# Performance work log

Measured on AMD Instinct MI355X. Metric: run time of the kernel, lower is better.

## Reference

```python
import jax, jax.numpy as jnp
import numpy as np

EPS = 2e-5
NCG = 51  # int(64 / 1.25)

def _conv1d(x, w, d):
    # x: [B,C,L], w: [Co,Ci,K]; dilated 1D conv, SAME padding
    return jax.lax.conv_general_dilated(x, w, window_strides=(1,), padding='SAME',
                                        rhs_dilation=(d,), dimension_numbers=('NCH', 'OIH', 'NCH'))

def _lift(x, w, n_h=9):
    # GConvRdG: lift R1 -> R1xR+; scale h=2^s realized as kernel dilation, 1/h normalization
    return jnp.stack([_conv1d(x, w, 2 ** s) / (2.0 ** s) for s in range(n_h)], axis=2)

def _gg(x, w):
    # GConvGG on [B,C,H,L]; w: [Co,Ci,Nk,K]; h_crop: H_out = H - Nk + 1.
    # Output scale s mixes input scales s..s+Nk-1, each with spatial dilation 2^(s+i).
    Nk, H = w.shape[2], x.shape[2]
    outs = []
    for s in range(H - Nk + 1):
        acc = None
        for i in range(Nk):
            d = 2 ** (s + i)
            t = _conv1d(x[:, :, s + i, :], w[:, :, i, :], d) / float(d)
            acc = t if acc is None else acc + t
        outs.append(acc)
    return jnp.stack(outs, axis=2)

def _bn(x, g, b):
    # training-mode BatchNorm2d over [B,C,H,L], per-channel stats
    m = jnp.mean(x, axis=(0, 2, 3), keepdims=True)
    v = jnp.var(x, axis=(0, 2, 3), keepdims=True)
    return (x - m) * jax.lax.rsqrt(v + EPS) * g[None, :, None, None] + b[None, :, None, None]

def _pool4(x):
    # max_pooling_R1: kernel 4 stride 4 over spatial axis
    B, C, H, L = x.shape
    return jnp.max(x.reshape(B, C, H, L // 4, 4), axis=-1)

def _forward(x, w1, w2, w3, w4, w5, w6, w7, w8, w9, w10, w11,
             g1, b1, g2, b2, g3, b3, g4, b4, g5, b5, g6, b6, g7, b7, g8, b8, g9, b9, g10, b10):
    r = jax.nn.relu
    out = _lift(x, w1)                      # [B,51,9,L]
    out = _pool4(out)
    out = r(_bn(out, g1, b1))
    out = _pool4(out)
    out = r(_bn(_gg(out, w2), g2, b2))      # H 9->7
    out = r(_bn(_gg(out, w3), g3, b3))
    out = _pool4(out)
    out = r(_bn(_gg(out, w4), g4, b4))      # 7->5
    out = r(_bn(_gg(out, w5), g5, b5))
    out = _pool4(out)
    out = r(_bn(_gg(out, w6), g6, b6))      # 5->3
    out = r(_bn(_gg(out, w7), g7, b7))
    out = r(_bn(_gg(out, w8), g8, b8))
    out = _pool4(out)
    out = r(_bn(_gg(out, w9), g9, b9))      # 3->1
    out = r(_bn(_gg(out, w10), g10, b10))
    out = jnp.mean(out, axis=-1, keepdims=True)   # global mean over space -> [B,408,1,1]
    out = _gg(out, w11)                     # 1x1 classifier -> [B,10,1,1]
    out = jnp.max(out, axis=-2)             # max over h axis -> [B,10,1]
    return out.reshape(out.shape[0], 10)

def setup_inputs():
    key = jax.random.key(0)
    ks = jax.random.split(key, 16)
    c = NCG
    def w(k, shape):
        fan_in = float(np.prod(shape[1:]))
        return jax.random.normal(k, shape, jnp.float32) * fan_in ** -0.5
    inp = {
        'x': jax.random.normal(ks[0], (8, 1, 32768), jnp.float32),
        'w1': w(ks[1], (c, 1, 79)),
        'w2': w(ks[2], (c, c, 3, 3)),
        'w3': w(ks[3], (c, c, 1, 3)),
        'w4': w(ks[4], (2 * c, c, 3, 3)),
        'w5': w(ks[5], (2 * c, 2 * c, 1, 3)),
        'w6': w(ks[6], (4 * c, 2 * c, 3, 3)),
        'w7': w(ks[7], (4 * c, 4 * c, 1, 3)),
        'w8': w(ks[8], (4 * c, 4 * c, 1, 3)),
        'w9': w(ks[9], (8 * c, 4 * c, 3, 3)),
        'w10': w(ks[10], (8 * c, 8 * c, 1, 3)),
        'w11': w(ks[11], (10, 8 * c, 1, 1)),
    }
    widths = [c, c, c, 2 * c, 2 * c, 4 * c, 4 * c, 4 * c, 8 * c, 8 * c]
    for i, cw in enumerate(widths, 1):
        inp['g%d' % i] = jnp.ones((cw,), jnp.float32)
        inp['b%d' % i] = jnp.zeros((cw,), jnp.float32)
    return inp

def reference(x, w1, w2, w3, w4, w5, w6, w7, w8, w9, w10, w11,
              g1, b1, g2, b2, g3, b3, g4, b4, g5, b5, g6, b6, g7, b7, g8, b8, g9, b9, g10, b10):
    return _forward(x, w1, w2, w3, w4, w5, w6, w7, w8, w9, w10, w11,
                    g1, b1, g2, b2, g3, b3, g4, b4, g5, b5, g6, b6, g7, b7, g8, b8, g9, b9, g10, b10)
```

## Files before the change

### kernel.cpp

```cpp
#include <hip/hip_runtime.h>
#include <hip/hip_bf16.h>

#define EPSBN 2e-5f

typedef __attribute__((ext_vector_type(8))) short short8v;
typedef __attribute__((ext_vector_type(4))) float f32x4;

__device__ inline unsigned short f2bf(float f) {
  unsigned u = __float_as_uint(f);
  unsigned r = (u + 0x7FFFu + ((u >> 16) & 1u)) >> 16;
  return (unsigned short)r;
}
__device__ inline float bf2f(unsigned short h) {
  return __uint_as_float(((unsigned)h) << 16);
}

template <int CTRL>
__device__ inline float dpp_radd(float v) {
  int r = __builtin_amdgcn_update_dpp(0, __float_as_int(v), CTRL, 0xf, 0xf,
                                      true);
  return v + __int_as_float(r);
}

constexpr int XPADL = 9984;
constexpr int XPADR = 14336;
constexpr int PROW = XPADL + 32768 + XPADR;

__global__ __launch_bounds__(256) void pad_x_kernel(const float* __restrict__ x,
                                                    unsigned* __restrict__ xp) {
  int i = blockIdx.x * 256 + threadIdx.x;
  if (i >= 8 * PROW) return;
  int b = i / PROW;
  int pos = i - b * PROW - XPADL;
  float v = (pos >= 0 && pos < 32768) ? x[b * 32768 + pos] : 0.f;
  unsigned u = __float_as_uint(v);
  unsigned h = u >> 16;
  float lof = v - __uint_as_float(u & 0xffff0000u);
  unsigned lo = __float_as_uint(lof) >> 16;
  xp[i] = (h << 16) | lo;
}

__global__ __launch_bounds__(256) void pad_pair_kernel(
    const unsigned* __restrict__ xp, unsigned* __restrict__ xpH,
    unsigned* __restrict__ xpL) {
  const int i = blockIdx.x * 256 + threadIdx.x;
  if (i >= PROW) return;
  const int sb = blockIdx.y;
  const int s = sb >> 3;
  const int b = sb & 7;
  const int d = 1 << s;
  const unsigned* row = xp + b * PROW;
  unsigned u0 = row[i];
  unsigned u1 = (i + d < PROW) ? row[i + d] : 0u;
  size_t o = (size_t)sb * PROW + i;
  xpH[o] = (u0 >> 16) | (u1 & 0xffff0000u);
  xpL[o] = (u0 & 0xffffu) | (u1 << 16);
}

__global__ __launch_bounds__(256) void pack_w1_kernel(
    const float* __restrict__ W, short* __restrict__ A) {
  int idx = blockIdx.x * 256 + threadIdx.x;
  if (idx >= 9 * 64 * 96) return;
  int s = idx / (64 * 96);
  int rem = idx - s * 64 * 96;
  int co = rem / 96;
  int k = rem - co * 96;
  float v = 0.f;
  if (co < 51 && k < 79)
    v = W[co * 79 + k] * __uint_as_float((unsigned)(127 - s) << 23);
  unsigned short hi = f2bf(v);
  unsigned short lo = f2bf(v - bf2f(hi));
  A[(size_t)s * 2 * 64 * 96 + co * 96 + k] = (short)hi;
  A[(size_t)s * 2 * 64 * 96 + 64 * 96 + co * 96 + k] = (short)lo;
}

__global__ __launch_bounds__(256) void lift_mfma_kernel(
    const unsigned* __restrict__ xpH, const unsigned* __restrict__ xpL,
    const short* __restrict__ Apk1, float* __restrict__ y1,
    float* __restrict__ part1) {
  constexpr int P = 104;
  const int bid = blockIdx.x;
  const int lc = (bid & 7) * 64 + (bid >> 3);
  const int s = blockIdx.y;
  const int b = blockIdx.z;
  const int d = 1 << s;
  const int l0 = lc * 64;
  const int tid = threadIdx.x;
  const int lane = tid & 63;
  const int quad = lane >> 4;
  const int n0 = lane & 15;
  const int wv = tid >> 6;
  const int coBase = wv * 16;

  __shared__ __align__(16) short Bh[64 * P];
  __shared__ __align__(16) short Bl[64 * P];
  __shared__ float sCh[2][64];

  const int nB = tid & 63;
  const int rowW = ((nB & 3) << 4) | (nB >> 2);
  const int swzW = (nB & 3) << 3;
  const int ogu = __builtin_amdgcn_readfirstlane(tid >> 6);
  const unsigned* xqH = xpH + (size_t)(s * 8 + b) * PROW + XPADL + l0;
  const unsigned* xqL = xpL + (size_t)(s * 8 + b) * PROW + XPADL + l0;

#pragma unroll
  for (int r = 0; r < 3; ++r) {
    const int kb = (ogu + 4 * r) * 8;
    const int base = (kb - 39) * d;
    uint4 ph, pl;
    ph.x = xqH[base + nB];
    ph.y = xqH[base + 2 * d + nB];
    ph.z = xqH[base + 4 * d + nB];
    ph.w = xqH[base + 6 * d + nB];
    pl.x = xqL[base + nB];
    pl.y = xqL[base + 2 * d + nB];
    pl.z = xqL[base + 4 * d + nB];
    pl.w = xqL[base + 6 * d + nB];
    *(uint4*)(Bh + rowW * P + (kb ^ swzW)) = ph;
    *(uint4*)(Bl + rowW * P + (kb ^ swzW)) = pl;
  }

  const short* ApkS = Apk1 + (size_t)s * 2 * 64 * 96;
  const short* arowH = ApkS + (coBase + n0) * 96;
  const short* arowL = arowH + 64 * 96;

  __syncthreads();

  f32x4 acc[4];
#pragma unroll
  for (int t = 0; t < 4; ++t) acc[t] = (f32x4){0.f, 0.f, 0.f, 0.f};

#pragma unroll
  for (int ks = 0; ks < 3; ++ks) {
    short8v ah = *(const short8v*)(arowH + ks * 32 + quad * 8);
    short8v al = *(const short8v*)(arowL + ks * 32 + quad * 8);
#pragma unroll
    for (int t = 0; t < 4; ++t) {
      const int n = n0 + 16 * t;
      const int off = (ks * 32 + quad * 8) ^ (t << 3);
      short8v bh = *(const short8v*)(Bh + n * P + off);
      short8v bl = *(const short8v*)(Bl + n * P + off);
      acc[t] = __builtin_amdgcn_mfma_f32_16x16x32_bf16(ah, bh, acc[t], 0, 0, 0);
      acc[t] = __builtin_amdgcn_mfma_f32_16x16x32_bf16(ah, bl, acc[t], 0, 0, 0);
      acc[t] = __builtin_amdgcn_mfma_f32_16x16x32_bf16(al, bh, acc[t], 0, 0, 0);
    }
  }

#pragma unroll
  for (int reg = 0; reg < 4; ++reg) {
    const int co = coBase + quad * 4 + reg;
    float po = fmaxf(fmaxf(acc[0][reg], acc[1][reg]),
                     fmaxf(acc[2][reg], acc[3][reg]));
    const bool valid = (co < 51);
    if (valid) {
      y1[(((size_t)b * 51 + co) * 9 + s) * 8192 + (l0 >> 2) + n0] = po;
    }
    float us = valid ? po : 0.f;
    float sq = us * us;
    us = dpp_radd<0x128>(us);
    sq = dpp_radd<0x128>(sq);
    us = dpp_radd<0x124>(us);
    sq = dpp_radd<0x124>(sq);
    us = dpp_radd<0x122>(us);
    sq = dpp_radd<0x122>(sq);
    us = dpp_radd<0x121>(us);
    sq = dpp_radd<0x121>(sq);
    if (n0 == 0) {
      sCh[0][co] = us;
      sCh[1][co] = sq;
    }
  }
  __syncthreads();
  if (tid < 51) {
    float* pp = part1 + (size_t)lc * 128;
    atomicAdd(&pp[tid], sCh[0][tid]);
    atomicAdd(&pp[64 + tid], sCh[1][tid]);
  }
}

__global__ __launch_bounds__(128) void reduce_stats1_kernel(
    const float* __restrict__ p, float* __restrict__ st) {
  const int t = threadIdx.x;
  if (t >= 102) return;
  const int k0 = blockIdx.x * 64;
  const int off = (t < 51) ? t : (64 + t - 51);
  float s = 0.f;
  for (int k = k0; k < k0 + 64; ++k) s += p[k * 128 + off];
  atomicAdd(&st[(t < 51) ? t : (512 + t - 51)], s);
}

__global__ __launch_bounds__(256) void stats_kernel(
    const float* __restrict__ Y, float* __restrict__ st, int C, int HL,
    int NS) {
  const int c = blockIdx.x, b = blockIdx.y, z = blockIdx.z;
  const int slice = HL / NS;
  const float* p = Y + ((size_t)b * C + c) * HL + (size_t)z * slice;
  float s = 0.f, q = 0.f;
  for (int i = threadIdx.x; i < slice; i += 256) {
    float v = p[i];
    s += v;
    q += v * v;
  }
#pragma unroll
  for (int off = 32; off > 0; off >>= 1) {
    s += __shfl_down(s, off, 64);
    q += __shfl_down(q, off, 64);
  }
  __shared__ float ls[4], lq[4];
  const int wid = threadIdx.x >> 6, lane = threadIdx.x & 63;
  if (lane == 0) { ls[wid] = s; lq[wid] = q; }
  __syncthreads();
  if (threadIdx.x == 0) {
    atomicAdd(&st[c], ls[0] + ls[1] + ls[2] + ls[3]);
    atomicAdd(&st[512 + c], lq[0] + lq[1] + lq[2] + lq[3]);
  }
}

__global__ __launch_bounds__(256) void reduce_parts_kernel(
    const float* __restrict__ p, float* __restrict__ y, int n, int stride,
    int ns) {
  int i = blockIdx.x * 256 + threadIdx.x;
  if (i >= n) return;
  float s = 0.f;
  for (int k = 0; k < ns; ++k) s += p[(size_t)k * stride + i];
  y[i] = s;
}

__global__ __launch_bounds__(256) void bnrelu_pool_kernel(
    const float* __restrict__ Y, const float* __restrict__ st,
    const float* __restrict__ g, const float* __restrict__ bb,
    float* __restrict__ Z, int C, int H, int Lin, float invN,
    unsigned int total) {
  unsigned int idx = blockIdx.x * 256u + threadIdx.x;
  if (idx >= total) return;
  const unsigned int Lo = (unsigned int)(Lin >> 2);
  unsigned int lo = idx % Lo;
  unsigned int r1 = idx / Lo;
  unsigned int h = r1 % (unsigned int)H;
  unsigned int r2 = r1 / (unsigned int)H;
  unsigned int c = r2 % (unsigned int)C;
  unsigned int b = r2 / (unsigned int)C;
  float m = st[c] * invN;
  float v = st[512 + c] * invN - m * m;
  float sc = g[c] * rsqrtf(v + EPSBN);
  float bi = bb[c] - m * sc;
  const float* p = Y + (((size_t)b * C + c) * H + h) * Lin + 4u * lo;
  float a0 = p[0] * sc + bi, a1 = p[1] * sc + bi;
  float a2 = p[2] * sc + bi, a3 = p[3] * sc + bi;
  float r = fmaxf(fmaxf(a0, a1), fmaxf(a2, a3));
  Z[idx] = fmaxf(r, 0.f);
}

__global__ __launch_bounds__(256) void bnrelu_pool_bf16_kernel(
    const float* __restrict__ Y, const float* __restrict__ st,
    const float* __restrict__ g, const float* __restrict__ bb,
    unsigned short* __restrict__ Z, int C, int H, int Lin, float invN,
    unsigned int total) {
  unsigned int idx = blockIdx.x * 256u + threadIdx.x;
  if (idx >= total) return;
  const unsigned int Lo = (unsigned int)(Lin >> 2);
  unsigned int lo = idx % Lo;
  unsigned int r1 = idx / Lo;
  unsigned int h = r1 % (unsigned int)H;
  unsigned int r2 = r1 / (unsigned int)H;
  unsigned int c = r2 % (unsigned int)C;
  unsigned int b = r2 / (unsigned int)C;
  float m = st[c] * invN;
  float v = st[512 + c] * invN - m * m;
  float sc = g[c] * rsqrtf(v + EPSBN);
  float bi = bb[c] - m * sc;
  const float* p = Y + (((size_t)b * C + c) * H + h) * Lin + 4u * lo;
  float a0 = p[0] * sc + bi, a1 = p[1] * sc + bi;
  float a2 = p[2] * sc + bi, a3 = p[3] * sc + bi;
  float r = fmaxf(fmaxf(a0, a1), fmaxf(a2, a3));
  Z[idx] = f2bf(fmaxf(r, 0.f));
}

__global__ __launch_bounds__(256) void bnrelu_kernel(
    const float* __restrict__ Y, const float* __restrict__ st,
    const float* __restrict__ g, const float* __restrict__ bb,
    float* __restrict__ A, int C, int HL, float invN, unsigned int total) {
  unsigned int idx = blockIdx.x * 256u + threadIdx.x;
  if (idx >= total) return;
  unsigned int c = (idx / (unsigned int)HL) % (unsigned int)C;
  float m = st[c] * invN;
  float v = st[512 + c] * invN - m * m;
  float sc = g[c] * rsqrtf(v + EPSBN);
  float bi = bb[c] - m * sc;
  A[idx] = fmaxf(fmaf(Y[idx], sc, bi), 0.f);
}

__global__ __launch_bounds__(256) void bnrelu_bf16_kernel(
    const float* __restrict__ Y, const float* __restrict__ st,
    const float* __restrict__ g, const float* __restrict__ bb,
    unsigned short* __restrict__ A, int C, int HL, float invN,
    unsigned int total) {
  unsigned int idx = blockIdx.x * 256u + threadIdx.x;
  if (idx >= total) return;
  unsigned int c = (idx / (unsigned int)HL) % (unsigned int)C;
  float m = st[c] * invN;
  float v = st[512 + c] * invN - m * m;
  float sc = g[c] * rsqrtf(v + EPSBN);
  float bi = bb[c] - m * sc;
  A[idx] = f2bf(fmaxf(fmaf(Y[idx], sc, bi), 0.f));
}

__global__ __launch_bounds__(256) void pack_w2_kernel(
    const float* __restrict__ W, short* __restrict__ A, int Co, int KTOT,
    int KPAD, int COPAD, int NS, int nk3) {
  int idx = blockIdx.x * 256 + threadIdx.x;
  const int CK = COPAD * KPAD;
  if (idx >= NS * CK) return;
  int s = idx / CK;
  int rem = idx - s * CK;
  int co = rem / KPAD;
  int kk = rem - co * KPAD;
  float v = 0.f;
  if (co < Co && kk < KTOT) {
    int i = (kk % nk3) / 3;
    float scale = __uint_as_float((unsigned)(127 - (s + i)) << 23);
    v = W[co * KTOT + kk] * scale;
  }
  unsigned short hi = f2bf(v);
  unsigned short lo = f2bf(v - bf2f(hi));
  A[(size_t)s * 2 * CK + co * KPAD + kk] = (short)hi;
  A[(size_t)s * 2 * CK + CK + co * KPAD + kk] = (short)lo;
}

template <int NKv, int LT>
__global__ __launch_bounds__(256) void gg_mfma5_kernel(
    const unsigned short* __restrict__ X, const short* __restrict__ Apk,
    float* __restrict__ Y, int Ci, int Co, int Hin, int L, int nL, int KTOT,
    int KPAD, int COPAD) {
  constexpr int T = LT / 16;
  constexpr int KO = 256 / LT;
  constexpr int RIT = 8 / KO;

  const int bx = blockIdx.x;
  const int lc = bx % nL;
  const int cog = bx / nL;
  const int s = blockIdx.y;
  const int b = blockIdx.z;
  const int Hout = Hin - NKv + 1;
  const int l0 = lc * LT;
  const int tid = threadIdx.x;
  const int lane = tid & 63;
  const int quad = lane >> 4;
  const int m0 = lane & 15;
  const int wv = tid >> 6;
  const int coBase = cog * 64 + wv * 16;

  __shared__ __align__(16) short Bh[LT * 72];
  __shared__ int roT[1024];
  __shared__ int shT[1024];

  for (int kk = tid; kk < KPAD; kk += 256) {
    int ro = 0, sh = -(1 << 30);
    if (kk < KTOT) {
      int ci = kk / (3 * NKv);
      int rem = kk - ci * (3 * NKv);
      int i = rem / 3;
      int k = rem - 3 * i;
      ro = (ci * Hin + s + i) * L;
      sh = (k - 1) * (1 << (s + i));
    }
    roT[kk] = ro;
    shT[kk] = sh;
  }
  __syncthreads();

  f32x4 acc[T];
#pragma unroll
  for (int t = 0; t < T; ++t) acc[t] = (f32x4){0.f, 0.f, 0.f, 0.f};

  const short* ApkS = Apk + (size_t)s * 2 * COPAD * KPAD;
  const short* arowH = ApkS + (size_t)(coBase + m0) * KPAD;
  const short* arowL = arowH + (size_t)COPAD * KPAD;
  const unsigned short* Xb = X + (size_t)b * Ci * Hin * L;

  const int lB = tid & (LT - 1);
  const int oc0 = tid / LT;
  const int nch = (KTOT + 63) >> 6;

  uint4 v0[RIT], v1[RIT], v2[RIT];
  auto gather = [&](int c0, uint4 (&pk)[RIT]) {
#pragma unroll
    for (int r = 0; r < RIT; ++r) {
      const int oct = oc0 + KO * r;
      const int kkb = (c0 << 6) + oct * 8;
      unsigned w[8];
#pragma unroll
      for (int j = 0; j < 8; ++j) {
        const int kk = kkb + j;
        const int pos = l0 + lB + shT[kk];
        const int posc = min(max(pos, 0), L - 1);
        unsigned u = (unsigned)Xb[roT[kk] + posc];
        w[j] = ((unsigned)pos < (unsigned)L) ? u : 0u;
      }
      pk[r].x = w[0] | (w[1] << 16);
      pk[r].y = w[2] | (w[3] << 16);
      pk[r].z = w[4] | (w[5] << 16);
      pk[r].w = w[6] | (w[7] << 16);
    }
  };

  gather(0, v0);
  if (nch > 1) gather(1, v1);
  for (int c0 = 0; c0 < nch; ++c0) {
#pragma unroll
    for (int r = 0; r < RIT; ++r)
      *(uint4*)(Bh + lB * 72 + (oc0 + KO * r) * 8) = v0[r];
    if (c0 + 2 < nch) gather(c0 + 2, v2);
    const int a0 = (c0 << 6) + quad * 8;
    short8v ah0 = *(const short8v*)(arowH + a0);
    short8v al0 = *(const short8v*)(arowL + a0);
    short8v ah1 = *(const short8v*)(arowH + a0 + 32);
    short8v al1 = *(const short8v*)(arowL + a0 + 32);
    __syncthreads();
#pragma unroll
    for (int t = 0; t < T; ++t) {
      const int l = m0 + 16 * t;
      short8v b0 = *(const short8v*)(Bh + l * 72 + quad * 8);
      short8v b1 = *(const short8v*)(Bh + l * 72 + 32 + quad * 8);
      acc[t] = __builtin_amdgcn_mfma_f32_16x16x32_bf16(ah0, b0, acc[t], 0, 0, 0);
      acc[t] = __builtin_amdgcn_mfma_f32_16x16x32_bf16(al0, b0, acc[t], 0, 0, 0);
      acc[t] = __builtin_amdgcn_mfma_f32_16x16x32_bf16(ah1, b1, acc[t], 0, 0, 0);
      acc[t] = __builtin_amdgcn_mfma_f32_16x16x32_bf16(al1, b1, acc[t], 0, 0, 0);
    }
    __syncthreads();
#pragma unroll
    for (int r = 0; r < RIT; ++r) {
      v0[r] = v1[r];
      v1[r] = v2[r];
    }
  }

#pragma unroll
  for (int reg = 0; reg < 4; ++reg) {
    const int co = coBase + quad * 4 + reg;
    if (co < Co) {
      float* yp = Y + (((size_t)b * Co + co) * Hout + s) * L + l0;
#pragma unroll
      for (int t = 0; t < T; ++t) yp[m0 + 16 * t] = acc[t][reg];
    }
  }
}

template <int NK, int L, int COSUB, int UN>
__global__ __launch_bounds__(256) void gg_tail3_kernel(
    const float* __restrict__ X, const float* __restrict__ W,
    float* __restrict__ Y, int Ci, int Co, int Hin, int NSPLIT, int ciPer,
    int partStride) {
  const int l = threadIdx.x % L;
  const int cs = threadIdx.x / L;
  const int co = blockIdx.x * COSUB + cs;
  const int s = blockIdx.y / NSPLIT;
  const int seg = blockIdx.y % NSPLIT;
  const int b = blockIdx.z;
  const int Hout = Hin - NK + 1;
  const int ciBeg = seg * ciPer;
  const int ciEnd = min(Ci, ciBeg + ciPer);

  float acc[NK];
#pragma unroll
  for (int i = 0; i < NK; ++i) acc[i] = 0.f;

  const float* wbase = W + (size_t)co * Ci * NK * 3;
  const float* xbase = X + ((size_t)b * Ci * Hin + s) * L;

  int ci = ciBeg;
  for (; ci + UN <= ciEnd; ci += UN) {
    float xv[UN][NK][3];
#pragma unroll
    for (int u = 0; u < UN; ++u) {
      const float* xr = xbase + (size_t)(ci + u) * (Hin * L);
#pragma unroll
      for (int i = 0; i < NK; ++i) {
        const int d = 1 << (s + i);
        const float* row = xr + i * L;
        xv[u][i][0] = (l >= d) ? row[l - d] : 0.f;
        xv[u][i][1] = row[l];
        xv[u][i][2] = (l + d < L) ? row[l + d] : 0.f;
      }
    }
#pragma unroll
    for (int u = 0; u < UN; ++u) {
      const float* wp = wbase + (ci + u) * (NK * 3);
#pragma unroll
      for (int i = 0; i < NK; ++i)
        acc[i] = fmaf(wp[3 * i], xv[u][i][0],
                      fmaf(wp[3 * i + 1], xv[u][i][1],
                           fmaf(wp[3 * i + 2], xv[u][i][2], acc[i])));
    }
  }
  for (; ci < ciEnd; ++ci) {
    const float* xr = xbase + (size_t)ci * (Hin * L);
    const float* wp = wbase + ci * (NK * 3);
#pragma unroll
    for (int i = 0; i < NK; ++i) {
      const int d = 1 << (s + i);
      const float* row = xr + i * L;
      float xm = (l >= d) ? row[l - d] : 0.f;
      float xc = row[l];
      float xp = (l + d < L) ? row[l + d] : 0.f;
      acc[i] = fmaf(wp[3 * i], xm,
                    fmaf(wp[3 * i + 1], xc, fmaf(wp[3 * i + 2], xp, acc[i])));
    }
  }
  float out = 0.f;
#pragma unroll
  for (int i = 0; i < NK; ++i) {
    float invd = __uint_as_float((unsigned)(127 - (s + i)) << 23);
    out = fmaf(acc[i], invd, out);
  }
  Y[(size_t)seg * partStride + (((size_t)b * Co + co) * Hout + s) * L + l] =
      out;
}

__global__ __launch_bounds__(256) void final_kernel(
    const float* __restrict__ Y, const float* __restrict__ st,
    const float* __restrict__ g, const float* __restrict__ bb,
    const float* __restrict__ w11, float* __restrict__ out) {
  const int b = blockIdx.x;
  const int tid = threadIdx.x;
  __shared__ float tch[408];
  for (int c = tid; c < 408; c += 256) {
    float m = st[c] * (1.f / 256.f);
    float v = st[512 + c] * (1.f / 256.f) - m * m;
    float sc = g[c] * rsqrtf(v + EPSBN);
    float bi = bb[c] - m * sc;
    const float* p = Y + ((size_t)b * 408 + c) * 32;
    float ssum = 0.f;
#pragma unroll
    for (int l = 0; l < 32; ++l) ssum += fmaxf(p[l] * sc + bi, 0.f);
    tch[c] = ssum * (1.f / 32.f);
  }
  __syncthreads();
  if (tid < 10) {
    float ssum = 0.f;
    for (int c = 0; c < 408; ++c) ssum += w11[tid * 408 + c] * tch[c];
    out[b * 10 + tid] = ssum;
  }
}

extern "C" void kernel_launch(void* const* d_in, const int* in_sizes, int n_in,
                              void* d_out, int out_size, void* d_ws,
                              size_t ws_size, hipStream_t stream) {
  const float* x = (const float*)d_in[0];
  const float* w1 = (const float*)d_in[1];
  const float* w2 = (const float*)d_in[2];
  const float* w3 = (const float*)d_in[3];
  const float* w4 = (const float*)d_in[4];
  const float* w5 = (const float*)d_in[5];
  const float* w6 = (const float*)d_in[6];
  const float* w7 = (const float*)d_in[7];
  const float* w8 = (const float*)d_in[8];
  const float* w9 = (const float*)d_in[9];
  const float* w10 = (const float*)d_in[10];
  const float* w11 = (const float*)d_in[11];
  const float* gg[11];
  const float* bbv[11];
  for (int i = 1; i <= 10; ++i) {
    gg[i] = (const float*)d_in[12 + 2 * (i - 1)];
    bbv[i] = (const float*)d_in[12 + 2 * (i - 1) + 1];
  }

  float* ws = (float*)d_ws;
  const size_t AR0 = 0;
  const size_t AR1 = 30081024;
  const size_t STATS = 38900000;
  float* y1 = ws + AR0;
  unsigned* xpad = (unsigned*)(ws + AR1);
  short* apk1 = (short*)(ws + AR1 + 460800);
  unsigned* xpairH = (unsigned*)(ws + AR1 + 520000);
  unsigned* xpairL = (unsigned*)(ws + AR1 + 4630336);
  float* part1 = ws + AR1 + 8740672;
  unsigned short* z1b = (unsigned short*)(ws + AR1);
  unsigned short* a3b = (unsigned short*)(ws + AR1);
  unsigned short* z3b = (unsigned short*)(ws + AR1);
  unsigned short* a5b = (unsigned short*)(ws + AR1 + 1500000);
  unsigned short* z5b = (unsigned short*)(ws + AR1);
  unsigned short* a6b = (unsigned short*)(ws + AR1 + 522240);
  unsigned short* a7b = (unsigned short*)(ws + AR1 + 1148928);
  float* z8 = ws + AR1;
  float* a9 = ws + AR1 + 1775616;
  float* part9 = ws + AR1 + 1900000;
  float* part10 = ws + AR1 + 2400000;
  float* y2 = ws + AR0;
  float* y3 = ws + AR0 + 5849088;
  float* y4 = ws + AR0;
  float* y5 = ws + AR0 + 2088960;
  float* y6 = ws + AR0;
  float* y7 = ws + AR0 + 626688;
  float* y8 = ws + AR0 + 1253376;
  float* y9 = ws + AR0;
  float* y10 = ws + AR0 + 104448;
  short* apk2 = (short*)(ws + 12000000);
  short* apk3 = apk2 + 7 * 2 * 64 * 512;
  short* apk4 = apk3 + 7 * 2 * 64 * 192;
  short* apk5 = apk4 + 5 * 2 * 128 * 512;
  short* apk6 = apk5 + 5 * 2 * 128 * 320;
  short* apk7 = apk6 + 3 * 2 * 256 * 960;
  short* apk8 = apk7 + 3 * 2 * 256 * 640;
  float* st[11];
  for (int i = 1; i <= 10; ++i) st[i] = ws + STATS + (size_t)(i - 1) * 1024;

  hipMemsetAsync((void*)(ws + STATS), 0, 10 * 1024 * sizeof(float), stream);
  hipMemsetAsync((void*)part1, 0, 512 * 128 * sizeof(float), stream);

  pad_x_kernel<<<(8 * PROW + 255) / 256, 256, 0, stream>>>(x, xpad);
  pad_pair_kernel<<<dim3((PROW + 255) / 256, 72), 256, 0, stream>>>(
      xpad, xpairH, xpairL);
  pack_w1_kernel<<<(9 * 64 * 96 + 255) / 256, 256, 0, stream>>>(w1, apk1);
  lift_mfma_kernel<<<dim3(512, 9, 8), 256, 0, stream>>>(xpairH, xpairL, apk1,
                                                        y1, part1);
  reduce_stats1_kernel<<<8, 128, 0, stream>>>(part1, st[1]);
  {
    unsigned int tot = 8u * 51 * 9 * 2048;
    bnrelu_pool_bf16_kernel<<<(tot + 255) / 256, 256, 0, stream>>>(
        y1, st[1], gg[1], bbv[1], z1b, 51, 9, 8192, 1.f / 589824.f, tot);
  }
  pack_w2_kernel<<<(7 * 64 * 512 + 255) / 256, 256, 0, stream>>>(
      w2, apk2, 51, 459, 512, 64, 7, 9);
  pack_w2_kernel<<<(7 * 64 * 192 + 255) / 256, 256, 0, stream>>>(
      w3, apk3, 51, 153, 192, 64, 7, 3);
  pack_w2_kernel<<<(5 * 128 * 512 + 255) / 256, 256, 0, stream>>>(
      w4, apk4, 102, 459, 512, 128, 5, 9);
  pack_w2_kernel<<<(5 * 128 * 320 + 255) / 256, 256, 0, stream>>>(
      w5, apk5, 102, 306, 320, 128, 5, 3);
  pack_w2_kernel<<<(3 * 256 * 960 + 255) / 256, 256, 0, stream>>>(
      w6, apk6, 204, 918, 960, 256, 3, 9);
  pack_w2_kernel<<<(3 * 256 * 640 + 255) / 256, 256, 0, stream>>>(
      w7, apk7, 204, 612, 640, 256, 3, 3);
  pack_w2_kernel<<<(3 * 256 * 640 + 255) / 256, 256, 0, stream>>>(
      w8, apk8, 204, 612, 640, 256, 3, 3);
  gg_mfma5_kernel<3, 64><<<dim3(32, 7, 8), 256, 0, stream>>>(
      z1b, apk2, y2, 51, 51, 9, 2048, 32, 459, 512, 64);
  stats_kernel<<<dim3(51, 8, 4), 256, 0, stream>>>(y2, st[2], 51, 7 * 2048, 4);
  {
    unsigned int tot = 8u * 51 * 7 * 2048;
    bnrelu_bf16_kernel<<<(tot + 255) / 256, 256, 0, stream>>>(
        y2, st[2], gg[2], bbv[2], a3b, 51, 7 * 2048, 1.f / 114688.f, tot);
  }
  gg_mfma5_kernel<1, 64><<<dim3(32, 7, 8), 256, 0, stream>>>(
      a3b, apk3, y3, 51, 51, 7, 2048, 32, 153, 192, 64);
  stats_kernel<<<dim3(51, 8, 4), 256, 0, stream>>>(y3, st[3], 51, 7 * 2048, 4);
  {
    unsigned int tot = 8u * 51 * 7 * 512;
    bnrelu_pool_bf16_kernel<<<(tot + 255) / 256, 256, 0, stream>>>(
        y3, st[3], gg[3], bbv[3], z3b, 51, 7, 2048, 1.f / 114688.f, tot);
  }
  gg_mfma5_kernel<3, 32><<<dim3(32, 5, 8), 256, 0, stream>>>(
      z3b, apk4, y4, 51, 102, 7, 512, 16, 459, 512, 128);
  stats_kernel<<<dim3(102, 8, 2), 256, 0, stream>>>(y4, st[4], 102, 5 * 512,
                                                    2);
  {
    unsigned int tot = 8u * 102 * 5 * 512;
    bnrelu_bf16_kernel<<<(tot + 255) / 256, 256, 0, stream>>>(
        y4, st[4], gg[4], bbv[4], a5b, 102, 5 * 512, 1.f / 20480.f, tot);
  }
  gg_mfma5_kernel<1, 32><<<dim3(32, 5, 8), 256, 0, stream>>>(
      a5b, apk5, y5, 102, 102, 5, 512, 16, 306, 320, 128);
  stats_kernel<<<dim3(102, 8, 2), 256, 0, stream>>>(y5, st[5], 102, 5 * 512,
                                                    2);
  {
    unsigned int tot = 8u * 102 * 5 * 128;
    bnrelu_pool_bf16_kernel<<<(tot + 255) / 256, 256, 0, stream>>>(
        y5, st[5], gg[5], bbv[5], z5b, 102, 5, 512, 1.f / 20480.f, tot);
  }
  gg_mfma5_kernel<3, 32><<<dim3(16, 3, 8), 256, 0, stream>>>(
      z5b, apk6, y6, 102, 204, 5, 128, 4, 918, 960, 256);
  stats_kernel<<<dim3(204, 8, 1), 256, 0, stream>>>(y6, st[6], 204, 384, 1);
  {
    unsigned int tot = 8u * 204 * 3 * 128;
    bnrelu_bf16_kernel<<<(tot + 255) / 256, 256, 0, stream>>>(
        y6, st[6], gg[6], bbv[6], a6b, 204, 3 * 128, 1.f / 3072.f, tot);
  }
  gg_mfma5_kernel<1, 32><<<dim3(16, 3, 8), 256, 0, stream>>>(
      a6b, apk7, y7, 204, 204, 3, 128, 4, 612, 640, 256);
  stats_kernel<<<dim3(204, 8, 1), 256, 0, stream>>>(y7, st[7], 204, 384, 1);
  {
    unsigned int tot = 8u * 204 * 3 * 128;
    bnrelu_bf16_kernel<<<(tot + 255) / 256, 256, 0, stream>>>(
        y7, st[7], gg[7], bbv[7], a7b, 204, 3 * 128, 1.f / 3072.f, tot);
  }
  gg_mfma5_kernel<1, 32><<<dim3(16, 3, 8), 256, 0, stream>>>(
      a7b, apk8, y8, 204, 204, 3, 128, 4, 612, 640, 256);
  stats_kernel<<<dim3(204, 8, 1), 256, 0, stream>>>(y8, st[8], 204, 384, 1);
  {
    unsigned int tot = 8u * 204 * 3 * 32;
    bnrelu_pool_kernel<<<(tot + 255) / 256, 256, 0, stream>>>(
        y8, st[8], gg[8], bbv[8], z8, 204, 3, 128, 1.f / 3072.f, tot);
  }
  gg_tail3_kernel<3, 32, 8, 2><<<dim3(51, 4, 8), 256, 0, stream>>>(
      z8, w9, part9, 204, 408, 3, 4, 51, 104448);
  reduce_parts_kernel<<<(104448 + 255) / 256, 256, 0, stream>>>(
      part9, y9, 104448, 104448, 4);
  stats_kernel<<<dim3(408, 8, 1), 256, 0, stream>>>(y9, st[9], 408, 32, 1);
  {
    unsigned int tot = 8u * 408 * 32;
    bnrelu_kernel<<<(tot + 255) / 256, 256, 0, stream>>>(
        y9, st[9], gg[9], bbv[9], a9, 408, 32, 1.f / 256.f, tot);
  }
  gg_tail3_kernel<1, 32, 8, 8><<<dim3(51, 4, 8), 256, 0, stream>>>(
      a9, w10, part10, 408, 408, 1, 4, 102, 104448);
  reduce_parts_kernel<<<(104448 + 255) / 256, 256, 0, stream>>>(
      part10, y10, 104448, 104448, 4);
  stats_kernel<<<dim3(408, 8, 1), 256, 0, stream>>>(y10, st[10], 408, 32, 1);
  final_kernel<<<dim3(8), 256, 0, stream>>>(y10, st[10], gg[10], bbv[10], w11,
                                            (float*)d_out);
}
```

Baseline: 686.7 us.

## Fuse BatchNorm statistics into MFMA conv epilogue with slotted atomic partials

The MFMA group-conv kernel now accumulates per-channel sum and sum-of-squares in its epilogue using DPP row reductions and shared memory. It atomically adds them into 8 slotted partial buffers keyed by the L-chunk index. The BN+ReLU(+pool) kernels sum those 8 slots per element to build scale and bias. This removes seven separate stats_kernel passes that re-read each conv output, at the cost of extra atomics, a barrier in the conv epilogue, and 16 redundant loads per element in the BN kernels.

Measured after the change: 607.5 us. 1.13x faster.

```diff
diff --git a/kernel.cpp b/kernel.cpp
--- a/kernel.cpp
+++ b/kernel.cpp
@@ -226,8 +226,24 @@
   y[i] = s;
 }
 
-__global__ __launch_bounds__(256) void bnrelu_pool_kernel(
-    const float* __restrict__ Y, const float* __restrict__ st,
+__device__ inline void parts_bn(const float* __restrict__ pp, unsigned c,
+                                float invN, const float* __restrict__ g,
+                                const float* __restrict__ bb, float& sc,
+                                float& bi) {
+  float ssum = 0.f, sqs = 0.f;
+#pragma unroll
+  for (int k = 0; k < 8; ++k) {
+    ssum += pp[k * 1024 + c];
+    sqs += pp[k * 1024 + 512 + c];
+  }
+  float m = ssum * invN;
+  float v = sqs * invN - m * m;
+  sc = g[c] * rsqrtf(v + EPSBN);
+  bi = bb[c] - m * sc;
+}
+
+__global__ __launch_bounds__(256) void bnrelu_pool_parts_kernel(
+    const float* __restrict__ Y, const float* __restrict__ pp,
     const float* __restrict__ g, const float* __restrict__ bb,
     float* __restrict__ Z, int C, int H, int Lin, float invN,
     unsigned int total) {
@@ -240,15 +256,36 @@
   unsigned int r2 = r1 / (unsigned int)H;
   unsigned int c = r2 % (unsigned int)C;
   unsigned int b = r2 / (unsigned int)C;
-  float m = st[c] * invN;
-  float v = st[512 + c] * invN - m * m;
-  float sc = g[c] * rsqrtf(v + EPSBN);
-  float bi = bb[c] - m * sc;
+  float sc, bi;
+  parts_bn(pp, c, invN, g, bb, sc, bi);
   const float* p = Y + (((size_t)b * C + c) * H + h) * Lin + 4u * lo;
   float a0 = p[0] * sc + bi, a1 = p[1] * sc + bi;
   float a2 = p[2] * sc + bi, a3 = p[3] * sc + bi;
   float r = fmaxf(fmaxf(a0, a1), fmaxf(a2, a3));
   Z[idx] = fmaxf(r, 0.f);
+}
+
+__global__ __launch_bounds__(256) void bnrelu_pool_bf16_parts_kernel(
+    const float* __restrict__ Y, const float* __restrict__ pp,
+    const float* __restrict__ g, const float* __restrict__ bb,
+    unsigned short* __restrict__ Z, int C, int H, int Lin, float invN,
+    unsigned int total) {
+  unsigned int idx = blockIdx.x * 256u + threadIdx.x;
+  if (idx >= total) return;
+  const unsigned int Lo = (unsigned int)(Lin >> 2);
+  unsigned int lo = idx % Lo;
+  unsigned int r1 = idx / Lo;
+  unsigned int h = r1 % (unsigned int)H;
+  unsigned int r2 = r1 / (unsigned int)H;
+  unsigned int c = r2 % (unsigned int)C;
+  unsigned int b = r2 / (unsigned int)C;
+  float sc, bi;
+  parts_bn(pp, c, invN, g, bb, sc, bi);
+  const float* p = Y + (((size_t)b * C + c) * H + h) * Lin + 4u * lo;
+  float a0 = p[0] * sc + bi, a1 = p[1] * sc + bi;
+  float a2 = p[2] * sc + bi, a3 = p[3] * sc + bi;
+  float r = fmaxf(fmaxf(a0, a1), fmaxf(a2, a3));
+  Z[idx] = f2bf(fmaxf(r, 0.f));
 }
 
 __global__ __launch_bounds__(256) void bnrelu_pool_bf16_kernel(
@@ -290,18 +327,16 @@
   A[idx] = fmaxf(fmaf(Y[idx], sc, bi), 0.f);
 }
 
-__global__ __launch_bounds__(256) void bnrelu_bf16_kernel(
-    const float* __restrict__ Y, const float* __restrict__ st,
+__global__ __launch_bounds__(256) void bnrelu_bf16_parts_kernel(
+    const float* __restrict__ Y, const float* __restrict__ pp,
     const float* __restrict__ g, const float* __restrict__ bb,
     unsigned short* __restrict__ A, int C, int HL, float invN,
     unsigned int total) {
   unsigned int idx = blockIdx.x * 256u + threadIdx.x;
   if (idx >= total) return;
   unsigned int c = (idx / (unsigned int)HL) % (unsigned int)C;
-  float m = st[c] * invN;
-  float v = st[512 + c] * invN - m * m;
-  float sc = g[c] * rsqrtf(v + EPSBN);
-  float bi = bb[c] - m * sc;
+  float sc, bi;
+  parts_bn(pp, c, invN, g, bb, sc, bi);
   A[idx] = f2bf(fmaxf(fmaf(Y[idx], sc, bi), 0.f));
 }
 
@@ -330,8 +365,8 @@
 template <int NKv, int LT>
 __global__ __launch_bounds__(256) void gg_mfma5_kernel(
     const unsigned short* __restrict__ X, const short* __restrict__ Apk,
-    float* __restrict__ Y, int Ci, int Co, int Hin, int L, int nL, int KTOT,
-    int KPAD, int COPAD) {
+    float* __restrict__ Y, float* __restrict__ part, int Ci, int Co, int Hin,
+    int L, int nL, int KTOT, int KPAD, int COPAD) {
   constexpr int T = LT / 16;
   constexpr int KO = 256 / LT;
   constexpr int RIT = 8 / KO;
@@ -353,6 +388,7 @@
   __shared__ __align__(16) short Bh[LT * 72];
   __shared__ int roT[1024];
   __shared__ int shT[1024];
+  __shared__ float sCh[2][64];
 
   for (int kk = tid; kk < KPAD; kk += 256) {
     int ro = 0, sh = -(1 << 30);
@@ -438,10 +474,37 @@
 #pragma unroll
   for (int reg = 0; reg < 4; ++reg) {
     const int co = coBase + quad * 4 + reg;
+    float ss = 0.f, sq = 0.f;
     if (co < Co) {
       float* yp = Y + (((size_t)b * Co + co) * Hout + s) * L + l0;
 #pragma unroll
-      for (int t = 0; t < T; ++t) yp[m0 + 16 * t] = acc[t][reg];
+      for (int t = 0; t < T; ++t) {
+        float v = acc[t][reg];
+        yp[m0 + 16 * t] = v;
+        ss += v;
+        sq = fmaf(v, v, sq);
+      }
+    }
+    ss = dpp_radd<0x128>(ss);
+    sq = dpp_radd<0x128>(sq);
+    ss = dpp_radd<0x124>(ss);
+    sq = dpp_radd<0x124>(sq);
+    ss = dpp_radd<0x122>(ss);
+    sq = dpp_radd<0x122>(sq);
+    ss = dpp_radd<0x121>(ss);
+    sq = dpp_radd<0x121>(sq);
+    if (m0 == 0) {
+      sCh[0][wv * 16 + quad * 4 + reg] = ss;
+      sCh[1][wv * 16 + quad * 4 + reg] = sq;
+    }
+  }
+  __syncthreads();
+  if (tid < 64) {
+    const int co = cog * 64 + tid;
+    if (co < Co) {
+      float* pp = part + (size_t)(lc & 7) * 1024;
+      atomicAdd(&pp[co], sCh[0][tid]);
+      atomicAdd(&pp[512 + co], sCh[1][tid]);
     }
   }
 }
@@ -604,9 +667,18 @@
   short* apk8 = apk7 + 3 * 2 * 256 * 640;
   float* st[11];
   for (int i = 1; i <= 10; ++i) st[i] = ws + STATS + (size_t)(i - 1) * 1024;
+  float* partg = ws + STATS + 10240;
+  float* part2 = partg;
+  float* part3 = partg + 8192;
+  float* part4 = partg + 2 * 8192;
+  float* part5 = partg + 3 * 8192;
+  float* part6 = partg + 4 * 8192;
+  float* part7 = partg + 5 * 8192;
+  float* part8 = partg + 6 * 8192;
 
   hipMemsetAsync((void*)(ws + STATS), 0, 10 * 1024 * sizeof(float), stream);
   hipMemsetAsync((void*)part1, 0, 512 * 128 * sizeof(float), stream);
+  hipMemsetAsync((void*)partg, 0, 7 * 8192 * sizeof(float), stream);
 
   pad_x_kernel<<<(8 * PROW + 255) / 256, 256, 0, stream>>>(x, xpad);
   pad_pair_kernel<<<dim3((PROW + 255) / 256, 72), 256, 0, stream>>>(
@@ -635,62 +707,53 @@
   pack_w2_kernel<<<(3 * 256 * 640 + 255) / 256, 256, 0, stream>>>(
       w8, apk8, 204, 612, 640, 256, 3, 3);
   gg_mfma5_kernel<3, 64><<<dim3(32, 7, 8), 256, 0, stream>>>(
-      z1b, apk2, y2, 51, 51, 9, 2048, 32, 459, 512, 64);
-  stats_kernel<<<dim3(51, 8, 4), 256, 0, stream>>>(y2, st[2], 51, 7 * 2048, 4);
+      z1b, apk2, y2, part2, 51, 51, 9, 2048, 32, 459, 512, 64);
   {
     unsigned int tot = 8u * 51 * 7 * 2048;
-    bnrelu_bf16_kernel<<<(tot + 255) / 256, 256, 0, stream>>>(
-        y2, st[2], gg[2], bbv[2], a3b, 51, 7 * 2048, 1.f / 114688.f, tot);
+    bnrelu_bf16_parts_kernel<<<(tot + 255) / 256, 256, 0, stream>>>(
+        y2, part2, gg[2], bbv[2], a3b, 51, 7 * 2048, 1.f / 114688.f, tot);
   }
   gg_mfma5_kernel<1, 64><<<dim3(32, 7, 8), 256, 0, stream>>>(
-      a3b, apk3, y3, 51, 51, 7, 2048, 32, 153, 192, 64);
-  stats_kernel<<<dim3(51, 8, 4), 256, 0, stream>>>(y3, st[3], 51, 7 * 2048, 4);
+      a3b, apk3, y3, part3, 51, 51, 7, 2048, 32, 153, 192, 64);
   {
     unsigned int tot = 8u * 51 * 7 * 512;
-    bnrelu_pool_bf16_kernel<<<(tot + 255) / 256, 256, 0, stream>>>(
-        y3, st[3], gg[3], bbv[3], z3b, 51, 7, 2048, 1.f / 114688.f, tot);
+    bnrelu_pool_bf16_parts_kernel<<<(tot + 255) / 256, 256, 0, stream>>>(
+        y3, part3, gg[3], bbv[3], z3b, 51, 7, 2048, 1.f / 114688.f, tot);
   }
   gg_mfma5_kernel<3, 32><<<dim3(32, 5, 8), 256, 0, stream>>>(
-      z3b, apk4, y4, 51, 102, 7, 512, 16, 459, 512, 128);
-  stats_kernel<<<dim3(102, 8, 2), 256, 0, stream>>>(y4, st[4], 102, 5 * 512,
-                                                    2);
+      z3b, apk4, y4, part4, 51, 102, 7, 512, 16, 459, 512, 128);
   {
     unsigned int tot = 8u * 102 * 5 * 512;
-    bnrelu_bf16_kernel<<<(tot + 255) / 256, 256, 0, stream>>>(
-        y4, st[4], gg[4], bbv[4], a5b, 102, 5 * 512, 1.f / 20480.f, tot);
+    bnrelu_bf16_parts_kernel<<<(tot + 255) / 256, 256, 0, stream>>>(
+        y4, part4, gg[4], bbv[4], a5b, 102, 5 * 512, 1.f / 20480.f, tot);
   }
   gg_mfma5_kernel<1, 32><<<dim3(32, 5, 8), 256, 0, stream>>>(
-      a5b, apk5, y5, 102, 102, 5, 512, 16, 306, 320, 128);
-  stats_kernel<<<dim3(102, 8, 2), 256, 0, stream>>>(y5, st[5], 102, 5 * 512,
-                                                    2);
+      a5b, apk5, y5, part5, 102, 102, 5, 512, 16, 306, 320, 128);
   {
     unsigned int tot = 8u * 102 * 5 * 128;
-    bnrelu_pool_bf16_kernel<<<(tot + 255) / 256, 256, 0, stream>>>(
-        y5, st[5], gg[5], bbv[5], z5b, 102, 5, 512, 1.f / 20480.f, tot);
+    bnrelu_pool_bf16_parts_kernel<<<(tot + 255) / 256, 256, 0, stream>>>(
+        y5, part5, gg[5], bbv[5], z5b, 102, 5, 512, 1.f / 20480.f, tot);
   }
   gg_mfma5_kernel<3, 32><<<dim3(16, 3, 8), 256, 0, stream>>>(
-      z5b, apk6, y6, 102, 204, 5, 128, 4, 918, 960, 256);
-  stats_kernel<<<dim3(204, 8, 1), 256, 0, stream>>>(y6, st[6], 204, 384, 1);
+      z5b, apk6, y6, part6, 102, 204, 5, 128, 4, 918, 960, 256);
   {
     unsigned int tot = 8u * 204 * 3 * 128;
-    bnrelu_bf16_kernel<<<(tot + 255) / 256, 256, 0, stream>>>(
-        y6, st[6], gg[6], bbv[6], a6b, 204, 3 * 128, 1.f / 3072.f, tot);
+    bnrelu_bf16_parts_kernel<<<(tot + 255) / 256, 256, 0, stream>>>(
+        y6, part6, gg[6], bbv[6], a6b, 204, 3 * 128, 1.f / 3072.f, tot);
   }
   gg_mfma5_kernel<1, 32><<<dim3(16, 3, 8), 256, 0, stream>>>(
-      a6b, apk7, y7, 204, 204, 3, 128, 4, 612, 640, 256);
-  stats_kernel<<<dim3(204, 8, 1), 256, 0, stream>>>(y7, st[7], 204, 384, 1);
+      a6b, apk7, y7, part7, 204, 204, 3, 128, 4, 612, 640, 256);
   {
     unsigned int tot = 8u * 204 * 3 * 128;
-    bnrelu_bf16_kernel<<<(tot + 255) / 256, 256, 0, stream>>>(
-        y7, st[7], gg[7], bbv[7], a7b, 204, 3 * 128, 1.f / 3072.f, tot);
+    bnrelu_bf16_parts_kernel<<<(tot + 255) / 256, 256, 0, stream>>>(
+        y7, part7, gg[7], bbv[7], a7b, 204, 3 * 128, 1.f / 3072.f, tot);
   }
   gg_mfma5_kernel<1, 32><<<dim3(16, 3, 8), 256, 0, stream>>>(
-      a7b, apk8, y8, 204, 204, 3, 128, 4, 612, 640, 256);
-  stats_kernel<<<dim3(204, 8, 1), 256, 0, stream>>>(y8, st[8], 204, 384, 1);
+      a7b, apk8, y8, part8, 204, 204, 3, 128, 4, 612, 640, 256);
   {
     unsigned int tot = 8u * 204 * 3 * 32;
-    bnrelu_pool_kernel<<<(tot + 255) / 256, 256, 0, stream>>>(
-        y8, st[8], gg[8], bbv[8], z8, 204, 3, 128, 1.f / 3072.f, tot);
+    bnrelu_pool_parts_kernel<<<(tot + 255) / 256, 256, 0, stream>>>(
+        y8, part8, gg[8], bbv[8], z8, 204, 3, 128, 1.f / 3072.f, tot);
   }
   gg_tail3_kernel<3, 32, 8, 2><<<dim3(51, 4, 8), 256, 0, stream>>>(
       z8, w9, part9, 204, 408, 3, 4, 51, 104448);
```
